# Kernel optimization log

Measured on AMD Instinct MI355X. Metric: run time of the kernel, lower is better.

The kernel has to match this reference:

```python
import jax, jax.numpy as jnp
from jax import lax
import numpy as np

B, T, LAT, HID, OUT, NC = 1024, 128, 128, 256, 128, 2
HODE = 128          # ODEFunc hidden width (hard-coded 128 in source)
H = LAT // 2        # LSTM hidden = latent_dim / 2


def setup_inputs() -> dict:
    key = jax.random.key(0)
    ks = jax.random.split(key, 8)
    s = 0.05
    f32 = jnp.float32
    return {
        "initial_state": jax.random.normal(ks[0], (B, LAT), f32),
        "time_steps": jnp.linspace(0.0, 1.0, T, dtype=f32),
        "ode_w1": jax.random.normal(ks[1], (HODE, LAT), f32) * s,
        "ode_b1": jnp.zeros((HODE,), f32),
        "ode_w2": jax.random.normal(ks[2], (LAT, HODE), f32) * s,
        "ode_b2": jnp.zeros((LAT,), f32),
        "l2h_w": jax.random.normal(ks[3], (HID, LAT), f32) * s,
        "l2h_b": jnp.zeros((HID,), f32),
        "h2o_w": jax.random.normal(ks[4], (OUT, HID), f32) * s,
        "h2o_b": jnp.zeros((OUT,), f32),
        "lstm_wih": jax.random.normal(ks[5], (4 * H, LAT), f32) * s,
        "lstm_whh": jax.random.normal(ks[6], (4 * H, H), f32) * s,
        "lstm_bih": jnp.zeros((4 * H,), f32),
        "lstm_bhh": jnp.zeros((4 * H,), f32),
        "fc2_w": jax.random.normal(ks[7], (NC, H), f32) * s,
        "fc2_b": jnp.zeros((NC,), f32),
    }


def reference(initial_state, time_steps, ode_w1, ode_b1, ode_w2, ode_b2,
              l2h_w, l2h_b, h2o_w, h2o_b,
              lstm_wih, lstm_whh, lstm_bih, lstm_bhh, fc2_w, fc2_b):
    def ode_f(y):  # Linear-ELU-Linear, time-independent
        return jax.nn.elu(y @ ode_w1.T + ode_b1) @ ode_w2.T + ode_b2

    def rk4_step(y, dt):
        k1 = ode_f(y)
        k2 = ode_f(y + 0.5 * dt * k1)
        k3 = ode_f(y + 0.5 * dt * k2)
        k4 = ode_f(y + dt * k3)
        y_new = y + (dt / 6.0) * (k1 + 2.0 * k2 + 2.0 * k3 + k4)
        return y_new, y_new

    dts = time_steps[1:] - time_steps[:-1]
    _, ys = lax.scan(rk4_step, initial_state, dts)
    zs = jnp.concatenate([initial_state[None], ys], axis=0)  # [T, B, LAT] = odeint output

    # torch: cat((initial_state.unsqueeze(0), zs)).permute(1,0,2) -> [B, T+1, LAT]
    input_lstm = jnp.concatenate([initial_state[None], zs], axis=0).transpose(1, 0, 2)

    # nn.LSTM is seq-first, so it scans dim0 (=B) with dim1 (=T+1) as its batch.
    h0 = jnp.zeros((input_lstm.shape[1], H), input_lstm.dtype)
    c0 = jnp.zeros_like(h0)

    def cell(carry, x):
        h, c = carry
        gates = x @ lstm_wih.T + lstm_bih + h @ lstm_whh.T + lstm_bhh
        i, f, g, o = jnp.split(gates, 4, axis=-1)  # torch gate order i,f,g,o
        c = jax.nn.sigmoid(f) * c + jax.nn.sigmoid(i) * jnp.tanh(g)
        h = jax.nn.sigmoid(o) * jnp.tanh(c)
        return (h, c), h

    _, lstm_hs = lax.scan(cell, (h0, c0), input_lstm)  # [B, T+1, H]
    lstm_out = lstm_hs[:, -1, :] @ fc2_w.T + fc2_b      # [B, NC]

    hs = zs @ l2h_w.T + l2h_b   # [T, B, HID]
    xs = hs @ h2o_w.T + h2o_b   # [T, B, OUT]
    return xs, lstm_out
```

## Files before the change

### kernel.cpp

```cpp
#include <hip/hip_runtime.h>


typedef short s16x8 __attribute__((ext_vector_type(8)));
typedef float f32x4 __attribute__((ext_vector_type(4)));
typedef _Float16 f16x2 __attribute__((ext_vector_type(2)));
typedef _Float16 f16x8 __attribute__((ext_vector_type(8)));

#define MFMA16(a, b, c) __builtin_amdgcn_mfma_f32_16x16x32_bf16((a), (b), (c), 0, 0, 0)

__device__ __forceinline__ void lds_barrier() {
  asm volatile("s_waitcnt lgkmcnt(0)\n\ts_barrier" ::: "memory");
}

__device__ __forceinline__ unsigned short f2bf(float x) {
  union { float f; unsigned u; } v; v.f = x;
  return (unsigned short)((v.u + 0x7FFFu + ((v.u >> 16) & 1u)) >> 16);
}

__device__ __forceinline__ int swz(int row, int col2) {
  return row * 256 + (col2 ^ ((row & 7) << 4));
}

__device__ __forceinline__ f16x8 cvt8(const float* p) {
  float4 a = *(const float4*)p, b = *(const float4*)(p + 4);
  return (f16x8){(_Float16)a.x, (_Float16)a.y, (_Float16)a.z, (_Float16)a.w,
                 (_Float16)b.x, (_Float16)b.y, (_Float16)b.z, (_Float16)b.w};
}

__global__ __launch_bounds__(128) void wf_kernel(
    const float* __restrict__ h2o, const float* __restrict__ l2h,
    const float* __restrict__ l2hb, const float* __restrict__ h2ob,
    unsigned short* __restrict__ wfo, float* __restrict__ bfo)
{
  const int o = (int)blockIdx.x, k = (int)threadIdx.x;
  float acc = 0.f;
  for (int h = 0; h < 256; ++h) acc = fmaf(h2o[o * 256 + h], l2h[h * 128 + k], acc);
  wfo[o * 128 + k] = f2bf(acc);
  __shared__ float red[128];
  red[k] = h2o[o * 256 + k] * l2hb[k] + h2o[o * 256 + 128 + k] * l2hb[128 + k];
  __syncthreads();
  for (int s = 64; s > 0; s >>= 1) {
    if (k < s) red[k] += red[k + s];
    __syncthreads();
  }
  if (k == 0) bfo[o] = red[0] + h2ob[o];
}

__global__ __launch_bounds__(256, 1) void ode_kernel(
    const float* __restrict__ init, const float* __restrict__ ts,
    const float* __restrict__ w1, const float* __restrict__ b1,
    const float* __restrict__ w2, const float* __restrict__ b2,
    const unsigned short* __restrict__ wf, const float* __restrict__ bfv_,
    float* __restrict__ xs, float* __restrict__ yfin)
{
  __shared__ __align__(16) unsigned char sY[4096];
  __shared__ __align__(16) unsigned char sH[4096];
  const int tid = (int)threadIdx.x;
  const int w = tid >> 6, lane = tid & 63;
  const int l15 = lane & 15, l4 = lane >> 4;
  const int rowbase = (int)blockIdx.x * 16;
  const int colbase = w * 32;

  s16x8 w1f[2][4], w2f[2][4], wff[2][4];
#pragma unroll
  for (int tc = 0; tc < 2; ++tc) {
    const int rj = colbase + 16 * tc + l15;
#pragma unroll
    for (int ks = 0; ks < 4; ++ks) {
      const int kb = ks * 32 + l4 * 8;
      s16x8 va, vb;
#pragma unroll
      for (int t = 0; t < 8; ++t) {
        va[t] = (short)f2bf(w1[rj * 128 + kb + t]);
        vb[t] = (short)f2bf(w2[rj * 128 + kb + t]);
      }
      w1f[tc][ks] = va; w2f[tc][ks] = vb;
      wff[tc][ks] = *(const s16x8*)(wf + rj * 128 + kb);
    }
  }
  float b1v[2], b2v[2], bv[2];
#pragma unroll
  for (int tc = 0; tc < 2; ++tc) {
    const int cc = colbase + 16 * tc + l15;
    b1v[tc] = b1[cc]; b2v[tc] = b2[cc]; bv[tc] = bfv_[cc];
  }

  int aOff[4];
#pragma unroll
  for (int ks = 0; ks < 4; ++ks) aOff[ks] = swz(l15, (ks * 32 + l4 * 8) * 2);
  int cOff[2][4];
#pragma unroll
  for (int tc = 0; tc < 2; ++tc)
#pragma unroll
    for (int r = 0; r < 4; ++r)
      cOff[tc][r] = swz(l4 * 4 + r, (colbase + 16 * tc + l15) * 2);

  float y0[2][4], yac[2][4];
#pragma unroll
  for (int tc = 0; tc < 2; ++tc)
#pragma unroll
    for (int r = 0; r < 4; ++r)
      y0[tc][r] = init[(rowbase + l4 * 4 + r) * 128 + colbase + 16 * tc + l15];

  {
    const int i = tid * 8;
    const int row = i >> 7, col = i & 127;
    union { unsigned short u[8]; s16x8 v; } p;
#pragma unroll
    for (int t = 0; t < 8; ++t) p.u[t] = f2bf(init[(rowbase + row) * 128 + col + t]);
    *(s16x8*)(sY + swz(row, col * 2)) = p.v;
  }
  __syncthreads();

  float* xsp = xs + (long)(rowbase + l4 * 4) * 128 + colbase + l15;
  const f32x4 fz = {0.f, 0.f, 0.f, 0.f};

  for (int s = 0; s < 127; ++s) {
    const float dt = ts[s + 1] - ts[s];
    const float c16 = dt * (1.f / 6.f), c13 = dt * (1.f / 3.f), ch = dt * 0.5f;
#pragma unroll
    for (int st = 0; st < 4; ++st) {
      f32x4 acc[2];
      acc[0] = fz; acc[1] = fz;
      if (st == 0) {
        s16x8 a[4];
#pragma unroll
        for (int ks = 0; ks < 4; ++ks) a[ks] = *(const s16x8*)(sY + aOff[ks]);
        f32x4 pa[2];
        pa[0] = fz; pa[1] = fz;
#pragma unroll
        for (int ks = 0; ks < 4; ++ks) {
          acc[0] = MFMA16(a[ks], w1f[0][ks], acc[0]);
          acc[1] = MFMA16(a[ks], w1f[1][ks], acc[1]);
          pa[0] = MFMA16(a[ks], wff[0][ks], pa[0]);
          pa[1] = MFMA16(a[ks], wff[1][ks], pa[1]);
        }
#pragma unroll
        for (int tc = 0; tc < 2; ++tc)
#pragma unroll
          for (int r = 0; r < 4; ++r)
            xsp[r * 128 + tc * 16] = pa[tc][r] + bv[tc];
        xsp += 131072;
      } else {
#pragma unroll
        for (int ks = 0; ks < 4; ++ks) {
          s16x8 a = *(const s16x8*)(sY + aOff[ks]);
          acc[0] = MFMA16(a, w1f[0][ks], acc[0]);
          acc[1] = MFMA16(a, w1f[1][ks], acc[1]);
        }
      }
#pragma unroll
      for (int tc = 0; tc < 2; ++tc)
#pragma unroll
        for (int r = 0; r < 4; ++r) {
          float v = acc[tc][r] + b1v[tc];
          v = v > 0.f ? v : (__expf(v) - 1.f);
          *(unsigned short*)(sH + cOff[tc][r]) = f2bf(v);
        }
      lds_barrier();
      f32x4 kc[2];
      kc[0] = fz; kc[1] = fz;
#pragma unroll
      for (int ks = 0; ks < 4; ++ks) {
        s16x8 a = *(const s16x8*)(sH + aOff[ks]);
        kc[0] = MFMA16(a, w2f[0][ks], kc[0]);
        kc[1] = MFMA16(a, w2f[1][ks], kc[1]);
      }
#pragma unroll
      for (int tc = 0; tc < 2; ++tc)
#pragma unroll
        for (int r = 0; r < 4; ++r) {
          const float kv = kc[tc][r] + b2v[tc];
          float yn;
          if (st == 0)      { yac[tc][r] = fmaf(c16, kv, y0[tc][r]);  yn = fmaf(ch, kv, y0[tc][r]); }
          else if (st == 1) { yac[tc][r] = fmaf(c13, kv, yac[tc][r]); yn = fmaf(ch, kv, y0[tc][r]); }
          else if (st == 2) { yac[tc][r] = fmaf(c13, kv, yac[tc][r]); yn = fmaf(dt, kv, y0[tc][r]); }
          else              { y0[tc][r]  = fmaf(c16, kv, yac[tc][r]); yn = y0[tc][r]; }
          *(unsigned short*)(sY + cOff[tc][r]) = f2bf(yn);
        }
      lds_barrier();
    }
  }
  {
    f32x4 pa[2];
    pa[0] = fz; pa[1] = fz;
#pragma unroll
    for (int ks = 0; ks < 4; ++ks) {
      s16x8 a = *(const s16x8*)(sY + aOff[ks]);
      pa[0] = MFMA16(a, wff[0][ks], pa[0]);
      pa[1] = MFMA16(a, wff[1][ks], pa[1]);
    }
#pragma unroll
    for (int tc = 0; tc < 2; ++tc)
#pragma unroll
      for (int r = 0; r < 4; ++r)
        xsp[r * 128 + tc * 16] = pa[tc][r] + bv[tc];
  }
#pragma unroll
  for (int tc = 0; tc < 2; ++tc)
#pragma unroll
    for (int r = 0; r < 4; ++r)
      yfin[(rowbase + l4 * 4 + r) * 128 + colbase + 16 * tc + l15] = y0[tc][r];
}

__global__ __launch_bounds__(256) void xw_kernel(
    const float* __restrict__ yfin, const float* __restrict__ wih,
    const float* __restrict__ bih, const float* __restrict__ bhh,
    float* __restrict__ XW4)
{
  const int t = (int)blockIdx.x, g = (int)threadIdx.x;
  const int q = g >> 6, j = g & 63;
  __shared__ __align__(16) float ys[128];
  if (g < 128) ys[g] = yfin[t * 128 + g];
  __syncthreads();
  float a0 = 0.f, a1 = 0.f, a2 = 0.f, a3 = 0.f;
#pragma unroll 8
  for (int k = 0; k < 32; ++k) {
    float4 wv = *(const float4*)(wih + g * 128 + 4 * k);
    float4 yv = *(const float4*)(ys + 4 * k);
    a0 = fmaf(wv.x, yv.x, a0); a1 = fmaf(wv.y, yv.y, a1);
    a2 = fmaf(wv.z, yv.z, a2); a3 = fmaf(wv.w, yv.w, a3);
  }
  XW4[t * 256 + j * 4 + q] = bih[g] + bhh[g] + ((a0 + a1) + (a2 + a3));
}

__global__ __launch_bounds__(128, 1) void lstm_kernel(
    const float* __restrict__ XW4,
    const float* __restrict__ whh,
    float* __restrict__ hsT)
{
  const int tid = (int)threadIdx.x;
  const int wv = tid >> 6, lane = tid & 63;
  const int odd = lane & 1;
  const int j = wv * 32 + (lane >> 1);
  const int rowA = odd * 128 + j;
  const int rowB = odd * 128 + 64 + j;

  __shared__ __align__(16) _Float16 hbuf[2][64];

  f16x8 wA[8], wB[8];
#pragma unroll
  for (int k = 0; k < 8; ++k) {
    wA[k] = cvt8(whh + rowA * 64 + 8 * k);
    wB[k] = cvt8(whh + rowB * 64 + 8 * k);
  }

  const float Aa = odd ? 2.f : 1.f;
  const float Sa = odd ? -2.f : -1.f;
  const float Ba = odd ? -1.f : 0.f;

  if (tid < 64) hbuf[0][tid] = (_Float16)0.f;
  float c = 0.f;

  const float2* XW2 = (const float2*)XW4;
  const int pidx = j * 2 + odd;
  float2 xq[4];
#pragma unroll
  for (int i = 0; i < 4; ++i) xq[i] = XW2[i * 128 + pidx];
  lds_barrier();

  for (int tb = 0; tb < 256; ++tb) {
#pragma unroll
    for (int i = 0; i < 4; ++i) {
      const int t = tb * 4 + i;
      const int cur = i & 1;
      const float2 xw = xq[i];
      xq[i] = XW2[((t + 4) & 1023) * 128 + pidx];

      const f16x8* hb8 = (const f16x8*)hbuf[cur];
      float4 acA = {0.f, 0.f, 0.f, 0.f}, acB = {0.f, 0.f, 0.f, 0.f};
#pragma unroll
      for (int r = 0; r < 8; ++r) {
        const f16x8 v = hb8[r];
        const f16x2 p0 = __builtin_shufflevector(v, v, 0, 1);
        const f16x2 p1 = __builtin_shufflevector(v, v, 2, 3);
        const f16x2 p2 = __builtin_shufflevector(v, v, 4, 5);
        const f16x2 p3 = __builtin_shufflevector(v, v, 6, 7);
        acA.x = __builtin_amdgcn_fdot2(__builtin_shufflevector(wA[r], wA[r], 0, 1), p0, acA.x, false);
        acA.y = __builtin_amdgcn_fdot2(__builtin_shufflevector(wA[r], wA[r], 2, 3), p1, acA.y, false);
        acA.z = __builtin_amdgcn_fdot2(__builtin_shufflevector(wA[r], wA[r], 4, 5), p2, acA.z, false);
        acA.w = __builtin_amdgcn_fdot2(__builtin_shufflevector(wA[r], wA[r], 6, 7), p3, acA.w, false);
        acB.x = __builtin_amdgcn_fdot2(__builtin_shufflevector(wB[r], wB[r], 0, 1), p0, acB.x, false);
        acB.y = __builtin_amdgcn_fdot2(__builtin_shufflevector(wB[r], wB[r], 2, 3), p1, acB.y, false);
        acB.z = __builtin_amdgcn_fdot2(__builtin_shufflevector(wB[r], wB[r], 4, 5), p2, acB.z, false);
        acB.w = __builtin_amdgcn_fdot2(__builtin_shufflevector(wB[r], wB[r], 6, 7), p3, acB.w, false);
      }
      const float preA = xw.x + ((acA.x + acA.y) + (acA.z + acA.w));
      const float preB = xw.y + ((acB.x + acB.y) + (acB.z + acB.w));

      const float actA = fmaf(Aa, __builtin_amdgcn_rcpf(1.f + __expf(Sa * preA)), Ba);
      const float actB = __builtin_amdgcn_rcpf(1.f + __expf(-preB));

      const float tg = __shfl_xor(actA, 1);
      const float og = __shfl_xor(actB, 1);

      c = fmaf(actB, c, actA * tg);
      const float th = fmaf(2.f, __builtin_amdgcn_rcpf(1.f + __expf(-2.f * c)), -1.f);
      const float h = og * th;

      if (!odd) {
        hbuf[cur ^ 1][j] = (_Float16)h;
        hsT[j * 1024 + t] = h;
      }
      lds_barrier();
    }
  }
}

__global__ __launch_bounds__(256) void fc2_kernel(
    const float* __restrict__ hsT, const float* __restrict__ fw,
    const float* __restrict__ fb, float* __restrict__ lout)
{
  const int idx = (int)blockIdx.x * 256 + (int)threadIdx.x;
  const int n = idx >> 10, t = idx & 1023;
  float acc = fb[n];
#pragma unroll 8
  for (int j = 0; j < 64; ++j) acc = fmaf(fw[n * 64 + j], hsT[j * 1024 + t], acc);
  lout[t * 2 + n] = acc;
}

extern "C" void kernel_launch(void* const* d_in, const int* in_sizes, int n_in,
                              void* d_out, int out_size, void* d_ws, size_t ws_size,
                              hipStream_t stream) {
  const float* init  = (const float*)d_in[0];
  const float* ts    = (const float*)d_in[1];
  const float* ode_w1 = (const float*)d_in[2];
  const float* ode_b1 = (const float*)d_in[3];
  const float* ode_w2 = (const float*)d_in[4];
  const float* ode_b2 = (const float*)d_in[5];
  const float* l2h_w = (const float*)d_in[6];
  const float* l2h_b = (const float*)d_in[7];
  const float* h2o_w = (const float*)d_in[8];
  const float* h2o_b = (const float*)d_in[9];
  const float* wih   = (const float*)d_in[10];
  const float* whh   = (const float*)d_in[11];
  const float* bih   = (const float*)d_in[12];
  const float* bhh   = (const float*)d_in[13];
  const float* fc2w  = (const float*)d_in[14];
  const float* fc2b  = (const float*)d_in[15];

  char* ws = (char*)d_ws;
  float* XW4            = (float*)(ws);
  float* hsT            = (float*)(ws + 1048576);
  float* yfin           = (float*)(ws + 1310720);
  unsigned short* wfbuf = (unsigned short*)(ws + 1835008);
  float* bfused         = (float*)(ws + 1867776);

  float* xs   = (float*)d_out;
  float* lout = xs + 16777216;

  wf_kernel<<<128, 128, 0, stream>>>(h2o_w, l2h_w, l2h_b, h2o_b, wfbuf, bfused);
  ode_kernel<<<64, 256, 0, stream>>>(init, ts, ode_w1, ode_b1, ode_w2, ode_b2,
                                     wfbuf, bfused, xs, yfin);
  xw_kernel<<<1024, 256, 0, stream>>>(yfin, wih, bih, bhh, XW4);
  lstm_kernel<<<1, 128, 0, stream>>>(XW4, whh, hsT);
  fc2_kernel<<<8, 256, 0, stream>>>(hsT, fc2w, fc2b, lout);
}
```

Baseline: 762.3 us.

## Fuse input projection into ODE kernel and widen LSTM to one gate per lane

The LSTM input projection (final ODE state times W_ih plus biases) is now computed at the end of the ODE kernel from a shared-memory copy of each block's final states. This removes the separate xw kernel launch and the yfin round trip through global memory. The serial LSTM kernel now runs 256 threads, each computing one gate row instead of two, and combines the four gates through three lane shuffles. Each step therefore does half the dot-product work per thread, at the cost of more shuffles and selects on the critical recurrent path.

```diff
diff --git a/kernel.cpp b/kernel.cpp
--- a/kernel.cpp
+++ b/kernel.cpp
@@ -51,10 +51,13 @@
     const float* __restrict__ w1, const float* __restrict__ b1,
     const float* __restrict__ w2, const float* __restrict__ b2,
     const unsigned short* __restrict__ wf, const float* __restrict__ bfv_,
-    float* __restrict__ xs, float* __restrict__ yfin)
+    const float* __restrict__ wih, const float* __restrict__ bih,
+    const float* __restrict__ bhh,
+    float* __restrict__ xs, float* __restrict__ XW4)
 {
   __shared__ __align__(16) unsigned char sY[4096];
   __shared__ __align__(16) unsigned char sH[4096];
+  __shared__ __align__(16) float sYf[2048];
   const int tid = (int)threadIdx.x;
   const int w = tid >> 6, lane = tid & 63;
   const int l15 = lane & 15, l4 = lane >> 4;
@@ -200,63 +203,54 @@
   for (int tc = 0; tc < 2; ++tc)
 #pragma unroll
     for (int r = 0; r < 4; ++r)
-      yfin[(rowbase + l4 * 4 + r) * 128 + colbase + 16 * tc + l15] = y0[tc][r];
-}
-
-__global__ __launch_bounds__(256) void xw_kernel(
-    const float* __restrict__ yfin, const float* __restrict__ wih,
-    const float* __restrict__ bih, const float* __restrict__ bhh,
-    float* __restrict__ XW4)
-{
-  const int t = (int)blockIdx.x, g = (int)threadIdx.x;
-  const int q = g >> 6, j = g & 63;
-  __shared__ __align__(16) float ys[128];
-  if (g < 128) ys[g] = yfin[t * 128 + g];
-  __syncthreads();
-  float a0 = 0.f, a1 = 0.f, a2 = 0.f, a3 = 0.f;
+      sYf[(l4 * 4 + r) * 128 + colbase + 16 * tc + l15] = y0[tc][r];
+  lds_barrier();
+  {
+    const int g = tid;
+    const int q = g >> 6, j = g & 63;
+#pragma unroll 4
+    for (int tl = 0; tl < 16; ++tl) {
+      float a0 = 0.f, a1 = 0.f, a2 = 0.f, a3 = 0.f;
 #pragma unroll 8
-  for (int k = 0; k < 32; ++k) {
-    float4 wv = *(const float4*)(wih + g * 128 + 4 * k);
-    float4 yv = *(const float4*)(ys + 4 * k);
-    a0 = fmaf(wv.x, yv.x, a0); a1 = fmaf(wv.y, yv.y, a1);
-    a2 = fmaf(wv.z, yv.z, a2); a3 = fmaf(wv.w, yv.w, a3);
-  }
-  XW4[t * 256 + j * 4 + q] = bih[g] + bhh[g] + ((a0 + a1) + (a2 + a3));
-}
-
-__global__ __launch_bounds__(128, 1) void lstm_kernel(
+      for (int k = 0; k < 32; ++k) {
+        float4 wv = *(const float4*)(wih + g * 128 + 4 * k);
+        float4 yv = *(const float4*)(sYf + tl * 128 + 4 * k);
+        a0 = fmaf(wv.x, yv.x, a0); a1 = fmaf(wv.y, yv.y, a1);
+        a2 = fmaf(wv.z, yv.z, a2); a3 = fmaf(wv.w, yv.w, a3);
+      }
+      XW4[(rowbase + tl) * 256 + j * 4 + q] = bih[g] + bhh[g] + ((a0 + a1) + (a2 + a3));
+    }
+  }
+}
+
+__global__ __launch_bounds__(256, 1) void lstm_kernel(
     const float* __restrict__ XW4,
     const float* __restrict__ whh,
     float* __restrict__ hsT)
 {
   const int tid = (int)threadIdx.x;
-  const int wv = tid >> 6, lane = tid & 63;
-  const int odd = lane & 1;
-  const int j = wv * 32 + (lane >> 1);
-  const int rowA = odd * 128 + j;
-  const int rowB = odd * 128 + 64 + j;
+  const int L = tid & 63;
+  const int q = L & 3;
+  const int j = (tid >> 6) * 16 + (L >> 2);
+  const int row = q * 64 + j;
 
   __shared__ __align__(16) _Float16 hbuf[2][64];
 
-  f16x8 wA[8], wB[8];
-#pragma unroll
-  for (int k = 0; k < 8; ++k) {
-    wA[k] = cvt8(whh + rowA * 64 + 8 * k);
-    wB[k] = cvt8(whh + rowB * 64 + 8 * k);
-  }
-
-  const float Aa = odd ? 2.f : 1.f;
-  const float Sa = odd ? -2.f : -1.f;
-  const float Ba = odd ? -1.f : 0.f;
+  f16x8 wq[8];
+#pragma unroll
+  for (int k = 0; k < 8; ++k) wq[k] = cvt8(whh + row * 64 + 8 * k);
+
+  const float Aa = (q == 2) ? 2.f : 1.f;
+  const float Sa = (q == 2) ? -2.f : -1.f;
+  const float Ba = (q == 2) ? -1.f : 0.f;
 
   if (tid < 64) hbuf[0][tid] = (_Float16)0.f;
   float c = 0.f;
 
-  const float2* XW2 = (const float2*)XW4;
-  const int pidx = j * 2 + odd;
-  float2 xq[4];
-#pragma unroll
-  for (int i = 0; i < 4; ++i) xq[i] = XW2[i * 128 + pidx];
+  const int xwi = j * 4 + q;
+  float xq[4];
+#pragma unroll
+  for (int i = 0; i < 4; ++i) xq[i] = XW4[i * 256 + xwi];
   lds_barrier();
 
   for (int tb = 0; tb < 256; ++tb) {
@@ -264,41 +258,39 @@
     for (int i = 0; i < 4; ++i) {
       const int t = tb * 4 + i;
       const int cur = i & 1;
-      const float2 xw = xq[i];
-      xq[i] = XW2[((t + 4) & 1023) * 128 + pidx];
+      const float xw = xq[i];
+      xq[i] = XW4[((t + 4) & 1023) * 256 + xwi];
 
       const f16x8* hb8 = (const f16x8*)hbuf[cur];
-      float4 acA = {0.f, 0.f, 0.f, 0.f}, acB = {0.f, 0.f, 0.f, 0.f};
+      float4 ac = {0.f, 0.f, 0.f, 0.f};
 #pragma unroll
       for (int r = 0; r < 8; ++r) {
         const f16x8 v = hb8[r];
-        const f16x2 p0 = __builtin_shufflevector(v, v, 0, 1);
-        const f16x2 p1 = __builtin_shufflevector(v, v, 2, 3);
-        const f16x2 p2 = __builtin_shufflevector(v, v, 4, 5);
-        const f16x2 p3 = __builtin_shufflevector(v, v, 6, 7);
-        acA.x = __builtin_amdgcn_fdot2(__builtin_shufflevector(wA[r], wA[r], 0, 1), p0, acA.x, false);
-        acA.y = __builtin_amdgcn_fdot2(__builtin_shufflevector(wA[r], wA[r], 2, 3), p1, acA.y, false);
-        acA.z = __builtin_amdgcn_fdot2(__builtin_shufflevector(wA[r], wA[r], 4, 5), p2, acA.z, false);
-        acA.w = __builtin_amdgcn_fdot2(__builtin_shufflevector(wA[r], wA[r], 6, 7), p3, acA.w, false);
-        acB.x = __builtin_amdgcn_fdot2(__builtin_shufflevector(wB[r], wB[r], 0, 1), p0, acB.x, false);
-        acB.y = __builtin_amdgcn_fdot2(__builtin_shufflevector(wB[r], wB[r], 2, 3), p1, acB.y, false);
-        acB.z = __builtin_amdgcn_fdot2(__builtin_shufflevector(wB[r], wB[r], 4, 5), p2, acB.z, false);
-        acB.w = __builtin_amdgcn_fdot2(__builtin_shufflevector(wB[r], wB[r], 6, 7), p3, acB.w, false);
-      }
-      const float preA = xw.x + ((acA.x + acA.y) + (acA.z + acA.w));
-      const float preB = xw.y + ((acB.x + acB.y) + (acB.z + acB.w));
-
-      const float actA = fmaf(Aa, __builtin_amdgcn_rcpf(1.f + __expf(Sa * preA)), Ba);
-      const float actB = __builtin_amdgcn_rcpf(1.f + __expf(-preB));
-
-      const float tg = __shfl_xor(actA, 1);
-      const float og = __shfl_xor(actB, 1);
-
-      c = fmaf(actB, c, actA * tg);
+        ac.x = __builtin_amdgcn_fdot2(__builtin_shufflevector(wq[r], wq[r], 0, 1),
+                                      __builtin_shufflevector(v, v, 0, 1), ac.x, false);
+        ac.y = __builtin_amdgcn_fdot2(__builtin_shufflevector(wq[r], wq[r], 2, 3),
+                                      __builtin_shufflevector(v, v, 2, 3), ac.y, false);
+        ac.z = __builtin_amdgcn_fdot2(__builtin_shufflevector(wq[r], wq[r], 4, 5),
+                                      __builtin_shufflevector(v, v, 4, 5), ac.z, false);
+        ac.w = __builtin_amdgcn_fdot2(__builtin_shufflevector(wq[r], wq[r], 6, 7),
+                                      __builtin_shufflevector(v, v, 6, 7), ac.w, false);
+      }
+      const float pre = xw + ((ac.x + ac.y) + (ac.z + ac.w));
+      const float act = fmaf(Aa, __builtin_amdgcn_rcpf(1.f + __expf(Sa * pre)), Ba);
+
+      const float x1 = __shfl_xor(act, 1);
+      const float x2 = __shfl_xor(act, 2);
+      const float x3 = __shfl_xor(act, 3);
+      const float gi = (q == 0) ? act : (q == 1) ? x1 : (q == 2) ? x2 : x3;
+      const float gf = (q == 0) ? x1 : (q == 1) ? act : (q == 2) ? x3 : x2;
+      const float gg = (q == 0) ? x2 : (q == 1) ? x3 : (q == 2) ? act : x1;
+      const float go = (q == 0) ? x3 : (q == 1) ? x2 : (q == 2) ? x1 : act;
+
+      c = fmaf(gf, c, gi * gg);
       const float th = fmaf(2.f, __builtin_amdgcn_rcpf(1.f + __expf(-2.f * c)), -1.f);
-      const float h = og * th;
-
-      if (!odd) {
+      const float h = go * th;
+
+      if (q == 0) {
         hbuf[cur ^ 1][j] = (_Float16)h;
         hsT[j * 1024 + t] = h;
       }
@@ -342,17 +334,15 @@
   char* ws = (char*)d_ws;
   float* XW4            = (float*)(ws);
   float* hsT            = (float*)(ws + 1048576);
-  float* yfin           = (float*)(ws + 1310720);
-  unsigned short* wfbuf = (unsigned short*)(ws + 1835008);
-  float* bfused         = (float*)(ws + 1867776);
+  unsigned short* wfbuf = (unsigned short*)(ws + 1310720);
+  float* bfused         = (float*)(ws + 1343488);
 
   float* xs   = (float*)d_out;
   float* lout = xs + 16777216;
 
   wf_kernel<<<128, 128, 0, stream>>>(h2o_w, l2h_w, l2h_b, h2o_b, wfbuf, bfused);
   ode_kernel<<<64, 256, 0, stream>>>(init, ts, ode_w1, ode_b1, ode_w2, ode_b2,
-                                     wfbuf, bfused, xs, yfin);
-  xw_kernel<<<1024, 256, 0, stream>>>(yfin, wih, bih, bhh, XW4);
-  lstm_kernel<<<1, 128, 0, stream>>>(XW4, whh, hsT);
+                                     wfbuf, bfused, wih, bih, bhh, xs, XW4);
+  lstm_kernel<<<1, 256, 0, stream>>>(XW4, whh, hsT);
   fc2_kernel<<<8, 256, 0, stream>>>(hsT, fc2w, fc2b, lout);
 }
```

New measurement: 803.9 us. +5.5%, slower.
